# Kernel tuning notes

Hardware: AMD Instinct MI355X
Metric: run time of the kernel (lower is better)

## Reference

```python
import jax, jax.numpy as jnp
import numpy as np

B, T, E, HH, V = 64, 128, 256, 256, 50000  # HH = hidden_size // 2 per LTC level
DT = 1.0


def setup_inputs() -> dict:
    key = jax.random.key(0)
    ks = jax.random.split(key, 12)
    s_in = 1.0 / np.sqrt(E)
    s_rec = 1.0 / np.sqrt(HH)
    tokens = jax.random.randint(ks[0], (B, T), 0, V, dtype=jnp.int32)
    emb = jax.random.normal(ks[1], (V, E), jnp.float32) * 0.02
    W_in0 = jax.random.normal(ks[2], (HH, E), jnp.float32) * s_in
    W_rec0 = jax.random.normal(ks[3], (HH, HH), jnp.float32) * s_rec
    b0 = jnp.zeros((HH,), jnp.float32)
    tau0 = jax.random.uniform(ks[4], (HH,), jnp.float32)
    # NCP sparsity mask: keep prob = 1 - sparsity_level = 0.5
    mask0 = (jax.random.uniform(ks[5], (HH, HH)) > 0.5).astype(jnp.float32)
    W_in1 = jax.random.normal(ks[6], (HH, HH), jnp.float32) * s_rec
    W_rec1 = jax.random.normal(ks[7], (HH, HH), jnp.float32) * s_rec
    b1 = jnp.zeros((HH,), jnp.float32)
    tau1 = jax.random.uniform(ks[8], (HH,), jnp.float32)
    mask1 = (jax.random.uniform(ks[9], (HH, HH)) > 0.5).astype(jnp.float32)
    return {"tokens": tokens, "emb": emb,
            "W_in0": W_in0, "W_rec0": W_rec0, "b0": b0, "tau0": tau0, "mask0": mask0,
            "W_in1": W_in1, "W_rec1": W_rec1, "b1": b1, "tau1": tau1, "mask1": mask1}


def _ltc_scan(x_seq, W_in, W_rec, mask, b, tau_raw):
    """LTC Euler integration over time. x_seq: [B, T, D] -> [B, T, H]."""
    tau = jax.nn.softplus(tau_raw) + 0.1        # positive time constants [H]
    Wr = W_rec * mask                            # NCP sparse recurrent weights
    x_proj = jnp.einsum('btd,hd->bth', x_seq, W_in) + b  # precompute input drive
    h0 = jnp.zeros((x_seq.shape[0], W_rec.shape[0]), x_seq.dtype)

    def step(h, xp_t):
        pre = xp_t + h @ Wr.T
        h_new = h + DT * ((-h + jnp.tanh(pre)) / tau)
        return h_new, h_new

    _, hs = jax.lax.scan(step, h0, jnp.swapaxes(x_proj, 0, 1))  # [T, B, H]
    return jnp.swapaxes(hs, 0, 1)


def reference(tokens, emb, W_in0, W_rec0, b0, tau0, mask0,
              W_in1, W_rec1, b1, tau1, mask1):
    x = emb[tokens]                                   # [B, T, E]
    h0_seq = _ltc_scan(x, W_in0, W_rec0, mask0, b0, tau0)      # level 0: [B, T, HH]
    h1_seq = _ltc_scan(h0_seq, W_in1, W_rec1, mask1, b1, tau1)  # level 1: [B, T, HH]
    return jnp.concatenate([h0_seq, h1_seq], axis=-1)  # [B, T, 2*HH] = hidden_size
```

## Files before the change

kernel.cpp:

```cpp
#include <hip/hip_runtime.h>
#include <hip/hip_bf16.h>

#define B_ 64
#define T_ 128
#define E_ 256
#define H_ 256
#define OW_ 512
#define LP 264
#define MAGIC 0x5AD00000u

typedef unsigned short ushort_t;
typedef __attribute__((ext_vector_type(8))) short bf16x8;
typedef __attribute__((ext_vector_type(4))) float f32x4;

#define LGKM_BARRIER() asm volatile("s_waitcnt lgkmcnt(0)\n\ts_barrier" ::: "memory")
#define PIN_FRAG(x) asm volatile("" : "+v"(x))

__device__ __forceinline__ ushort_t f2bf(float f) {
    unsigned int x = __float_as_uint(f);
    unsigned int r = x + 0x7FFFu + ((x >> 16) & 1u);
    return (ushort_t)(r >> 16);
}
__device__ __forceinline__ float fast_tanh(float x) {
    float e = __expf(2.0f * x);
    return 1.0f - 2.0f * __builtin_amdgcn_rcpf(e + 1.0f);
}
__device__ __forceinline__ bf16x8 load_bfrag(const float* W, const float* M,
                                             size_t base) {
    float4 a = *(const float4*)(W + base);
    float4 b = *(const float4*)(W + base + 4);
    if (M) {
        float4 ma = *(const float4*)(M + base);
        float4 mb = *(const float4*)(M + base + 4);
        a.x *= ma.x; a.y *= ma.y; a.z *= ma.z; a.w *= ma.w;
        b.x *= mb.x; b.y *= mb.y; b.z *= mb.z; b.w *= mb.w;
    }
    union { bf16x8 v; ushort_t u[8]; } r;
    r.u[0] = f2bf(a.x); r.u[1] = f2bf(a.y); r.u[2] = f2bf(a.z); r.u[3] = f2bf(a.w);
    r.u[4] = f2bf(b.x); r.u[5] = f2bf(b.y); r.u[6] = f2bf(b.z); r.u[7] = f2bf(b.w);
    return r.v;
}

__device__ __forceinline__ int a_off(int r, int k) {
    return ((k >> 5) << 9) + (((k >> 3) & 3) << 7) + (r << 3) + (k & 7);
}

template<bool FUSE, bool WAIT>
__device__ __forceinline__ void scan_core(
    int grp, ushort_t (*hb)[4096],
    const float* xp, int xp_stride, int xp_col,
    float* hout, int out_col,
    const float* Wrec, const float* Wmask, const float* tau_raw,
    const float* Wf, const float* bfv, float* xf,
    unsigned int* flag, const unsigned int* projf)
{
    const int tid  = threadIdx.x;
    const int lane = tid & 63;
    const int wv   = tid >> 6;
    const int quad = lane >> 4;
    const int l15  = lane & 15;
    const int n0   = wv * 32;
    const int bg   = grp * 8;

    bf16x8 Bf[2][8];
    #pragma unroll
    for (int tc = 0; tc < 2; ++tc)
        #pragma unroll
        for (int kk = 0; kk < 8; ++kk)
            Bf[tc][kk] = load_bfrag(Wrec, Wmask,
                (size_t)(n0 + tc * 16 + l15) * H_ + kk * 32 + quad * 8);

    bf16x8 Bf2[2][8];
    float  b2[2] = {0.f, 0.f};
    if (FUSE) {
        #pragma unroll
        for (int tc = 0; tc < 2; ++tc) {
            b2[tc] = bfv[n0 + tc * 16 + l15];
            #pragma unroll
            for (int kk = 0; kk < 8; ++kk)
                Bf2[tc][kk] = load_bfrag(Wf, nullptr,
                    (size_t)(n0 + tc * 16 + l15) * H_ + kk * 32 + quad * 8);
        }
    }

    float inv_tau[2], h_prev[2][2];
    float xp_c[2][2], xp_n[2][2], xp_nn[2][2];
    #pragma unroll
    for (int tc = 0; tc < 2; ++tc) {
        inv_tau[tc] = 1.0f / (logf(1.0f + __expf(tau_raw[n0 + tc * 16 + l15])) + 0.1f);
        #pragma unroll
        for (int reg = 0; reg < 2; ++reg) {
            h_prev[tc][reg] = 0.0f;
            xp_c[tc][reg] = xp_n[tc][reg] = xp_nn[tc][reg] = 0.0f;
        }
    }

    int woff[2][2];
    #pragma unroll
    for (int tc = 0; tc < 2; ++tc)
        #pragma unroll
        for (int reg = 0; reg < 2; ++reg)
            woff[tc][reg] = a_off(quad * 4 + reg, n0 + tc * 16 + l15);
    const int ab = ((l15 & 2) == 0) ? (lane * 8) : 0;

    if (!WAIT) {
        if (FUSE && projf != nullptr) {
            if (tid < 8) {
                const unsigned p = (unsigned)(bg + tid);
                for (;;) {
                    unsigned v = __hip_atomic_load(&projf[p], __ATOMIC_ACQUIRE,
                                                   __HIP_MEMORY_SCOPE_AGENT);
                    if (v == MAGIC) break;
                    __builtin_amdgcn_s_sleep(2);
                }
            }
            __syncthreads();
        }
        #pragma unroll
        for (int tc = 0; tc < 2; ++tc)
            #pragma unroll
            for (int reg = 0; reg < 2; ++reg) {
                const int b = bg + quad * 2 + reg;
                const int c = n0 + tc * 16 + l15;
                xp_c[tc][reg] = xp[(size_t)(b * T_ + 0) * xp_stride + xp_col + c];
                xp_n[tc][reg] = xp[(size_t)(b * T_ + 1) * xp_stride + xp_col + c];
            }
    }

    for (int i = tid; i < 4096; i += 512)
        ((unsigned int*)&hb[0][0])[i] = 0u;
    __syncthreads();

    const int tmax = FUSE ? T_ : (T_ - 1);
    for (int t = 0; t <= tmax; ++t) {
        const int rb = t & 1;

        #pragma unroll
        for (int tc = 0; tc < 2; ++tc)
            #pragma unroll
            for (int kk = 0; kk < 8; ++kk) {
                PIN_FRAG(Bf[tc][kk]);
                if (FUSE) PIN_FRAG(Bf2[tc][kk]);
            }

        if (WAIT && t < T_ && (t & 7) == 0) {
            if (tid == 0) {
                const unsigned need = (unsigned)(t >> 3) + 1u;
                for (;;) {
                    unsigned d = __hip_atomic_load(flag, __ATOMIC_ACQUIRE,
                                                   __HIP_MEMORY_SCOPE_AGENT) - MAGIC;
                    if (d >= need && d <= 16u) break;
                    __builtin_amdgcn_s_sleep(2);
                }
            }
            __syncthreads();
            #pragma unroll
            for (int tc = 0; tc < 2; ++tc)
                #pragma unroll
                for (int reg = 0; reg < 2; ++reg) {
                    const int b = bg + quad * 2 + reg;
                    xp_c[tc][reg] = xp[(size_t)(b * T_ + t) * xp_stride + xp_col
                                       + n0 + tc * 16 + l15];
                }
        }

        bf16x8 Af[8];
        {
            const ushort_t* a0 = &hb[rb][0];
            #pragma unroll
            for (int kk = 0; kk < 8; ++kk)
                Af[kk] = *(const bf16x8*)(a0 + ab + kk * 512);
        }

        if (t < T_) {
            if (WAIT) {
                if ((t & 7) != 7 && t + 1 < T_) {
                    #pragma unroll
                    for (int tc = 0; tc < 2; ++tc)
                        #pragma unroll
                        for (int reg = 0; reg < 2; ++reg) {
                            const int b = bg + quad * 2 + reg;
                            xp_n[tc][reg] = xp[(size_t)(b * T_ + t + 1) * xp_stride
                                               + xp_col + n0 + tc * 16 + l15];
                        }
                }
            } else if (t + 2 < T_) {
                if (FUSE && projf != nullptr && ((t + 2) & 31) == 0) {
                    if (tid < 8) {
                        const unsigned p = (unsigned)(((t + 2) >> 5) * 64 + bg + tid);
                        for (;;) {
                            unsigned v = __hip_atomic_load(&projf[p],
                                                           __ATOMIC_ACQUIRE,
                                                           __HIP_MEMORY_SCOPE_AGENT);
                            if (v == MAGIC) break;
                            __builtin_amdgcn_s_sleep(2);
                        }
                    }
                    __syncthreads();
                }
                #pragma unroll
                for (int tc = 0; tc < 2; ++tc)
                    #pragma unroll
                    for (int reg = 0; reg < 2; ++reg) {
                        const int b = bg + quad * 2 + reg;
                        xp_nn[tc][reg] = xp[(size_t)(b * T_ + t + 2) * xp_stride
                                            + xp_col + n0 + tc * 16 + l15];
                    }
            }

            f32x4 acc[2] = {{0.f,0.f,0.f,0.f},{0.f,0.f,0.f,0.f}};
            #pragma unroll
            for (int kk = 0; kk < 8; ++kk)
                #pragma unroll
                for (int tc = 0; tc < 2; ++tc)
                    acc[tc] = __builtin_amdgcn_mfma_f32_16x16x32_bf16(
                        Af[kk], Bf[tc][kk], acc[tc], 0, 0, 0);

            #pragma unroll
            for (int tc = 0; tc < 2; ++tc) {
                const int c = n0 + tc * 16 + l15;
                #pragma unroll
                for (int reg = 0; reg < 2; ++reg) {
                    const int b = bg + quad * 2 + reg;
                    const float pre = xp_c[tc][reg] + acc[tc][reg];
                    const float hn  = h_prev[tc][reg]
                                    + (fast_tanh(pre) - h_prev[tc][reg]) * inv_tau[tc];
                    h_prev[tc][reg] = hn;
                    hb[rb ^ 1][woff[tc][reg]] = f2bf(hn);
                    hout[(size_t)(b * T_ + t) * OW_ + out_col + c] = hn;
                }
            }
            if (WAIT) {
                if ((t & 7) != 7) {
                    #pragma unroll
                    for (int tc = 0; tc < 2; ++tc)
                        #pragma unroll
                        for (int reg = 0; reg < 2; ++reg)
                            xp_c[tc][reg] = xp_n[tc][reg];
                }
            } else {
                #pragma unroll
                for (int tc = 0; tc < 2; ++tc)
                    #pragma unroll
                    for (int reg = 0; reg < 2; ++reg) {
                        xp_c[tc][reg] = xp_n[tc][reg];
                        xp_n[tc][reg] = xp_nn[tc][reg];
                    }
            }
        }

        if (FUSE && t > 0) {
            f32x4 acc2[2];
            #pragma unroll
            for (int tc = 0; tc < 2; ++tc)
                acc2[tc] = (f32x4){b2[tc], b2[tc], b2[tc], b2[tc]};
            #pragma unroll
            for (int kk = 0; kk < 8; ++kk)
                #pragma unroll
                for (int tc = 0; tc < 2; ++tc)
                    acc2[tc] = __builtin_amdgcn_mfma_f32_16x16x32_bf16(
                        Af[kk], Bf2[tc][kk], acc2[tc], 0, 0, 0);
            #pragma unroll
            for (int tc = 0; tc < 2; ++tc) {
                const int c = n0 + tc * 16 + l15;
                #pragma unroll
                for (int reg = 0; reg < 2; ++reg) {
                    const int b = bg + quad * 2 + reg;
                    __hip_atomic_store(&xf[(size_t)(b * T_ + t - 1) * H_ + c],
                                       acc2[tc][reg],
                                       __ATOMIC_RELAXED, __HIP_MEMORY_SCOPE_AGENT);
                }
            }
        }

        if (FUSE && t > 0 && (t & 7) == 0) {
            __syncthreads();
            if (tid == 0)
                __hip_atomic_store(flag, MAGIC + (unsigned)(t >> 3),
                                   __ATOMIC_RELEASE, __HIP_MEMORY_SCOPE_AGENT);
        } else if (t < tmax) {
            LGKM_BARRIER();
        }
    }
}

__device__ __forceinline__ void proj_body(
    int r0, const float* __restrict__ src, int src_stride, int src_col,
    const int* __restrict__ tok,
    const float* __restrict__ Wi, const float* __restrict__ bias,
    float* __restrict__ dst, int dst_stride, int dst_col,
    unsigned int* done, int done_idx)
{
    const int tid  = threadIdx.x;
    const int lane = tid & 63;
    const int wv   = tid >> 6;
    const int quad = lane >> 4;
    const int l15  = lane & 15;
    const int n0   = wv * 32;

    __shared__ __align__(16) ushort_t As[32][LP];

    bf16x8 Bf[2][8];
    float  bj[2];
    #pragma unroll
    for (int tc = 0; tc < 2; ++tc) {
        const int n = n0 + tc * 16 + l15;
        bj[tc] = bias[n];
        #pragma unroll
        for (int kk = 0; kk < 8; ++kk)
            Bf[tc][kk] = load_bfrag(Wi, nullptr, (size_t)n * H_ + kk * 32 + quad * 8);
    }

    {
        const int row = tid >> 4;
        const int seg = tid & 15;
        const size_t sb = (tok ? (size_t)tok[r0 + row] : (size_t)(r0 + row))
                          * src_stride + src_col + seg * 16;
        union { uint4 q[2]; ushort_t u[16]; } p;
        #pragma unroll
        for (int h = 0; h < 2; ++h) {
            float4 f0 = *(const float4*)(src + sb + h * 8);
            float4 f1 = *(const float4*)(src + sb + h * 8 + 4);
            p.u[h*8+0] = f2bf(f0.x); p.u[h*8+1] = f2bf(f0.y);
            p.u[h*8+2] = f2bf(f0.z); p.u[h*8+3] = f2bf(f0.w);
            p.u[h*8+4] = f2bf(f1.x); p.u[h*8+5] = f2bf(f1.y);
            p.u[h*8+6] = f2bf(f1.z); p.u[h*8+7] = f2bf(f1.w);
        }
        *(uint4*)&As[row][seg * 16]     = p.q[0];
        *(uint4*)&As[row][seg * 16 + 8] = p.q[1];
    }
    __syncthreads();

    #pragma unroll
    for (int rt = 0; rt < 2; ++rt) {
        bf16x8 Af[8];
        #pragma unroll
        for (int kk = 0; kk < 8; ++kk)
            Af[kk] = *(const bf16x8*)&As[rt * 16 + l15][kk * 32 + quad * 8];

        f32x4 acc[2] = {{bj[0],bj[0],bj[0],bj[0]}, {bj[1],bj[1],bj[1],bj[1]}};
        #pragma unroll
        for (int kk = 0; kk < 8; ++kk)
            #pragma unroll
            for (int tc = 0; tc < 2; ++tc)
                acc[tc] = __builtin_amdgcn_mfma_f32_16x16x32_bf16(
                    Af[kk], Bf[tc][kk], acc[tc], 0, 0, 0);

        #pragma unroll
        for (int tc = 0; tc < 2; ++tc) {
            const int c = n0 + tc * 16 + l15;
            #pragma unroll
            for (int reg = 0; reg < 4; ++reg) {
                const int r = r0 + rt * 16 + quad * 4 + reg;
                if (done)
                    __hip_atomic_store(&dst[(size_t)r * dst_stride + dst_col + c],
                                       acc[tc][reg],
                                       __ATOMIC_RELAXED, __HIP_MEMORY_SCOPE_AGENT);
                else
                    dst[(size_t)r * dst_stride + dst_col + c] = acc[tc][reg];
            }
        }
    }

    if (done) {
        __syncthreads();
        if (tid == 0)
            __hip_atomic_store(&done[done_idx], MAGIC,
                               __ATOMIC_RELEASE, __HIP_MEMORY_SCOPE_AGENT);
    }
}

__global__ __launch_bounds__(512, 1)
void ltc_all(const int* __restrict__ tokens, const float* __restrict__ emb,
             const float* __restrict__ Wi0, const float* __restrict__ b0v,
             const float* __restrict__ Wr0, const float* __restrict__ m0,
             const float* __restrict__ t0,
             const float* __restrict__ Wi1, const float* __restrict__ b1v,
             const float* __restrict__ Wr1, const float* __restrict__ m1,
             const float* __restrict__ t1,
             float* out, float* xf, unsigned int* flags, unsigned int* projf)
{
    __shared__ __align__(16) ushort_t hb[2][4096];
    if (blockIdx.x < 8)
        scan_core<true, false>(blockIdx.x, hb,
                               out, OW_, H_,
                               out, 0,
                               Wr0, m0, t0, Wi1, b1v, xf,
                               flags + blockIdx.x, projf);
    else if (blockIdx.x < 16)
        scan_core<false, true>(blockIdx.x - 8, hb,
                               xf, H_, 0,
                               out, H_,
                               Wr1, m1, t1, nullptr, nullptr, nullptr,
                               flags + blockIdx.x - 8, nullptr);
    else {
        const int p  = blockIdx.x - 16;
        const int r0 = (p & 63) * T_ + (p >> 6) * 32;
        proj_body(r0, emb, E_, 0, tokens, Wi0, b0v, out, OW_, H_, projf, p);
    }
}

__global__ __launch_bounds__(512, 1)
void ltc_dual(float* out,
              const float* __restrict__ Wr0, const float* __restrict__ m0,
              const float* __restrict__ t0,
              const float* __restrict__ Wi1, const float* __restrict__ b1v,
              const float* __restrict__ Wr1, const float* __restrict__ m1,
              const float* __restrict__ t1,
              float* xf, unsigned int* flags)
{
    __shared__ __align__(16) ushort_t hb[2][4096];
    if (blockIdx.x < 8)
        scan_core<true, false>(blockIdx.x, hb,
                               out, OW_, H_, out, 0,
                               Wr0, m0, t0, Wi1, b1v, xf,
                               flags + blockIdx.x, nullptr);
    else
        scan_core<false, true>(blockIdx.x - 8, hb,
                               xf, H_, 0, out, H_,
                               Wr1, m1, t1, nullptr, nullptr, nullptr,
                               flags + blockIdx.x - 8, nullptr);
}

__global__ __launch_bounds__(512, 1)
void ltc_single(const float* xp, int xp_stride, int xp_col,
                float* hout, int out_col,
                const float* __restrict__ Wr, const float* __restrict__ mk,
                const float* __restrict__ tu)
{
    __shared__ __align__(16) ushort_t hb[2][4096];
    scan_core<false, false>(blockIdx.x, hb, xp, xp_stride, xp_col,
                            hout, out_col, Wr, mk, tu,
                            nullptr, nullptr, nullptr, nullptr, nullptr);
}

__global__ __launch_bounds__(512, 2)
void proj_mfma(const float* __restrict__ src, int src_stride, int src_col,
               const int* __restrict__ tok,
               const float* __restrict__ Wi,
               const float* __restrict__ bias,
               float* __restrict__ dst, int dst_stride, int dst_col)
{
    proj_body(blockIdx.x * 32, src, src_stride, src_col, tok, Wi, bias,
              dst, dst_stride, dst_col, nullptr, 0);
}

extern "C" void kernel_launch(void* const* d_in, const int* in_sizes, int n_in,
                              void* d_out, int out_size, void* d_ws, size_t ws_size,
                              hipStream_t stream)
{
    const int*   tokens = (const int*)d_in[0];
    const float* emb    = (const float*)d_in[1];
    const float* W_in0  = (const float*)d_in[2];
    const float* W_rec0 = (const float*)d_in[3];
    const float* b0     = (const float*)d_in[4];
    const float* tau0   = (const float*)d_in[5];
    const float* mask0  = (const float*)d_in[6];
    const float* W_in1  = (const float*)d_in[7];
    const float* W_rec1 = (const float*)d_in[8];
    const float* b1     = (const float*)d_in[9];
    const float* tau1   = (const float*)d_in[10];
    const float* mask1  = (const float*)d_in[11];
    float* out = (float*)d_out;
    (void)in_sizes; (void)n_in; (void)out_size;

    const size_t xf_elems = (size_t)B_ * T_ * H_;
    const size_t xf_bytes = xf_elems * sizeof(float);

    if (ws_size >= xf_bytes + 64 + 1024) {
        float* xf = (float*)d_ws;
        unsigned int* flags = (unsigned int*)((char*)d_ws + xf_bytes);
        unsigned int* projf = (unsigned int*)((char*)d_ws + xf_bytes + 64);
        ltc_all<<<dim3(272), dim3(512), 0, stream>>>(
            tokens, emb, W_in0, b0, W_rec0, mask0, tau0,
            W_in1, b1, W_rec1, mask1, tau1, out, xf, flags, projf);
    } else if (ws_size >= xf_bytes + 64) {
        float* xf = (float*)d_ws;
        unsigned int* flags = (unsigned int*)((char*)d_ws + xf_bytes);
        proj_mfma<<<dim3(256), dim3(512), 0, stream>>>(
            emb, E_, 0, tokens, W_in0, b0, out, OW_, H_);
        ltc_dual<<<dim3(16), dim3(512), 0, stream>>>(
            out, W_rec0, mask0, tau0, W_in1, b1, W_rec1, mask1, tau1, xf, flags);
    } else {
        proj_mfma<<<dim3(256), dim3(512), 0, stream>>>(
            emb, E_, 0, tokens, W_in0, b0, out, OW_, H_);
        ltc_single<<<dim3(8), dim3(512), 0, stream>>>(
            out, OW_, H_, out, 0, W_rec0, mask0, tau0);
        proj_mfma<<<dim3(256), dim3(512), 0, stream>>>(
            out, OW_, 0, nullptr, W_in1, b1, out, OW_, H_);
        ltc_single<<<dim3(8), dim3(512), 0, stream>>>(
            out, OW_, H_, out, H_, W_rec1, mask1, tau1);
    }
}
```

Baseline: 262.2 us.

## Move level-1 input projection from level-0 scan into dedicated fuser blocks

The level-0 scan blocks no longer compute the W_in1 projection inline each timestep. Eight new fuser blocks wait for 8-step chunks of h0 and project them with MFMA into xf, which the level-1 scan then consumes. The embedding projection is also re-chunked so the first 8 timesteps are published first, letting the level-0 scan start sooner. This shortens the serial per-step critical path of the level-0 recurrence, at the cost of extra flag handshakes and re-reading h0 from global memory.

```diff
diff --git a/kernel.cpp b/kernel.cpp
--- a/kernel.cpp
+++ b/kernel.cpp
@@ -45,13 +45,12 @@
     return ((k >> 5) << 9) + (((k >> 3) & 3) << 7) + (r << 3) + (k & 7);
 }
 
-template<bool FUSE, bool WAIT>
+template<bool PUB, bool WAIT>
 __device__ __forceinline__ void scan_core(
     int grp, ushort_t (*hb)[4096],
     const float* xp, int xp_stride, int xp_col,
     float* hout, int out_col,
     const float* Wrec, const float* Wmask, const float* tau_raw,
-    const float* Wf, const float* bfv, float* xf,
     unsigned int* flag, const unsigned int* projf)
 {
     const int tid  = threadIdx.x;
@@ -70,19 +69,6 @@
             Bf[tc][kk] = load_bfrag(Wrec, Wmask,
                 (size_t)(n0 + tc * 16 + l15) * H_ + kk * 32 + quad * 8);
 
-    bf16x8 Bf2[2][8];
-    float  b2[2] = {0.f, 0.f};
-    if (FUSE) {
-        #pragma unroll
-        for (int tc = 0; tc < 2; ++tc) {
-            b2[tc] = bfv[n0 + tc * 16 + l15];
-            #pragma unroll
-            for (int kk = 0; kk < 8; ++kk)
-                Bf2[tc][kk] = load_bfrag(Wf, nullptr,
-                    (size_t)(n0 + tc * 16 + l15) * H_ + kk * 32 + quad * 8);
-        }
-    }
-
     float inv_tau[2], h_prev[2][2];
     float xp_c[2][2], xp_n[2][2], xp_nn[2][2];
     #pragma unroll
@@ -104,11 +90,11 @@
     const int ab = ((l15 & 2) == 0) ? (lane * 8) : 0;
 
     if (!WAIT) {
-        if (FUSE && projf != nullptr) {
+        if (PUB && projf != nullptr) {
             if (tid < 8) {
-                const unsigned p = (unsigned)(bg + tid);
                 for (;;) {
-                    unsigned v = __hip_atomic_load(&projf[p], __ATOMIC_ACQUIRE,
+                    unsigned v = __hip_atomic_load(&projf[bg + tid],
+                                                   __ATOMIC_ACQUIRE,
                                                    __HIP_MEMORY_SCOPE_AGENT);
                     if (v == MAGIC) break;
                     __builtin_amdgcn_s_sleep(2);
@@ -131,19 +117,16 @@
         ((unsigned int*)&hb[0][0])[i] = 0u;
     __syncthreads();
 
-    const int tmax = FUSE ? T_ : (T_ - 1);
-    for (int t = 0; t <= tmax; ++t) {
+    for (int t = 0; t < T_; ++t) {
         const int rb = t & 1;
 
         #pragma unroll
         for (int tc = 0; tc < 2; ++tc)
             #pragma unroll
-            for (int kk = 0; kk < 8; ++kk) {
+            for (int kk = 0; kk < 8; ++kk)
                 PIN_FRAG(Bf[tc][kk]);
-                if (FUSE) PIN_FRAG(Bf2[tc][kk]);
-            }
-
-        if (WAIT && t < T_ && (t & 7) == 0) {
+
+        if (WAIT && (t & 7) == 0) {
             if (tid == 0) {
                 const unsigned need = (unsigned)(t >> 3) + 1u;
                 for (;;) {
@@ -172,24 +155,26 @@
                 Af[kk] = *(const bf16x8*)(a0 + ab + kk * 512);
         }
 
-        if (t < T_) {
-            if (WAIT) {
-                if ((t & 7) != 7 && t + 1 < T_) {
+        if (WAIT) {
+            if ((t & 7) != 7 && t + 1 < T_) {
+                #pragma unroll
+                for (int tc = 0; tc < 2; ++tc)
                     #pragma unroll
-                    for (int tc = 0; tc < 2; ++tc)
-                        #pragma unroll
-                        for (int reg = 0; reg < 2; ++reg) {
-                            const int b = bg + quad * 2 + reg;
-                            xp_n[tc][reg] = xp[(size_t)(b * T_ + t + 1) * xp_stride
-                                               + xp_col + n0 + tc * 16 + l15];
-                        }
-                }
-            } else if (t + 2 < T_) {
-                if (FUSE && projf != nullptr && ((t + 2) & 31) == 0) {
+                    for (int reg = 0; reg < 2; ++reg) {
+                        const int b = bg + quad * 2 + reg;
+                        xp_n[tc][reg] = xp[(size_t)(b * T_ + t + 1) * xp_stride
+                                           + xp_col + n0 + tc * 16 + l15];
+                    }
+            }
+        } else if (t + 2 < T_) {
+            if (PUB && projf != nullptr) {
+                const int tp2 = t + 2;
+                const int w = (tp2 == 8) ? 1 : (tp2 == 32) ? 2
+                            : (tp2 == 64) ? 3 : (tp2 == 96) ? 4 : -1;
+                if (w >= 0) {
                     if (tid < 8) {
-                        const unsigned p = (unsigned)(((t + 2) >> 5) * 64 + bg + tid);
                         for (;;) {
-                            unsigned v = __hip_atomic_load(&projf[p],
+                            unsigned v = __hip_atomic_load(&projf[w * 64 + bg + tid],
                                                            __ATOMIC_ACQUIRE,
                                                            __HIP_MEMORY_SCOPE_AGENT);
                             if (v == MAGIC) break;
@@ -198,98 +183,78 @@
                     }
                     __syncthreads();
                 }
+            }
+            #pragma unroll
+            for (int tc = 0; tc < 2; ++tc)
+                #pragma unroll
+                for (int reg = 0; reg < 2; ++reg) {
+                    const int b = bg + quad * 2 + reg;
+                    xp_nn[tc][reg] = xp[(size_t)(b * T_ + t + 2) * xp_stride
+                                        + xp_col + n0 + tc * 16 + l15];
+                }
+        }
+
+        f32x4 acc[2] = {{0.f,0.f,0.f,0.f},{0.f,0.f,0.f,0.f}};
+        #pragma unroll
+        for (int kk = 0; kk < 8; ++kk)
+            #pragma unroll
+            for (int tc = 0; tc < 2; ++tc)
+                acc[tc] = __builtin_amdgcn_mfma_f32_16x16x32_bf16(
+                    Af[kk], Bf[tc][kk], acc[tc], 0, 0, 0);
+
+        #pragma unroll
+        for (int tc = 0; tc < 2; ++tc) {
+            const int c = n0 + tc * 16 + l15;
+            #pragma unroll
+            for (int reg = 0; reg < 2; ++reg) {
+                const int b = bg + quad * 2 + reg;
+                const float pre = xp_c[tc][reg] + acc[tc][reg];
+                const float hn  = h_prev[tc][reg]
+                                + (fast_tanh(pre) - h_prev[tc][reg]) * inv_tau[tc];
+                h_prev[tc][reg] = hn;
+                hb[rb ^ 1][woff[tc][reg]] = f2bf(hn);
+                if (PUB)
+                    __hip_atomic_store(&hout[(size_t)(b * T_ + t) * OW_ + out_col + c],
+                                       hn, __ATOMIC_RELAXED, __HIP_MEMORY_SCOPE_AGENT);
+                else
+                    hout[(size_t)(b * T_ + t) * OW_ + out_col + c] = hn;
+            }
+        }
+        if (WAIT) {
+            if ((t & 7) != 7) {
                 #pragma unroll
                 for (int tc = 0; tc < 2; ++tc)
                     #pragma unroll
-                    for (int reg = 0; reg < 2; ++reg) {
-                        const int b = bg + quad * 2 + reg;
-                        xp_nn[tc][reg] = xp[(size_t)(b * T_ + t + 2) * xp_stride
-                                            + xp_col + n0 + tc * 16 + l15];
-                    }
-            }
-
-            f32x4 acc[2] = {{0.f,0.f,0.f,0.f},{0.f,0.f,0.f,0.f}};
-            #pragma unroll
-            for (int kk = 0; kk < 8; ++kk)
-                #pragma unroll
-                for (int tc = 0; tc < 2; ++tc)
-                    acc[tc] = __builtin_amdgcn_mfma_f32_16x16x32_bf16(
-                        Af[kk], Bf[tc][kk], acc[tc], 0, 0, 0);
-
-            #pragma unroll
-            for (int tc = 0; tc < 2; ++tc) {
-                const int c = n0 + tc * 16 + l15;
+                    for (int reg = 0; reg < 2; ++reg)
+                        xp_c[tc][reg] = xp_n[tc][reg];
+            }
+        } else {
+            #pragma unroll
+            for (int tc = 0; tc < 2; ++tc)
                 #pragma unroll
                 for (int reg = 0; reg < 2; ++reg) {
-                    const int b = bg + quad * 2 + reg;
-                    const float pre = xp_c[tc][reg] + acc[tc][reg];
-                    const float hn  = h_prev[tc][reg]
-                                    + (fast_tanh(pre) - h_prev[tc][reg]) * inv_tau[tc];
-                    h_prev[tc][reg] = hn;
-                    hb[rb ^ 1][woff[tc][reg]] = f2bf(hn);
-                    hout[(size_t)(b * T_ + t) * OW_ + out_col + c] = hn;
-                }
-            }
-            if (WAIT) {
-                if ((t & 7) != 7) {
-                    #pragma unroll
-                    for (int tc = 0; tc < 2; ++tc)
-                        #pragma unroll
-                        for (int reg = 0; reg < 2; ++reg)
-                            xp_c[tc][reg] = xp_n[tc][reg];
-                }
-            } else {
-                #pragma unroll
-                for (int tc = 0; tc < 2; ++tc)
-                    #pragma unroll
-                    for (int reg = 0; reg < 2; ++reg) {
-                        xp_c[tc][reg] = xp_n[tc][reg];
-                        xp_n[tc][reg] = xp_nn[tc][reg];
-                    }
-            }
-        }
-
-        if (FUSE && t > 0) {
-            f32x4 acc2[2];
-            #pragma unroll
-            for (int tc = 0; tc < 2; ++tc)
-                acc2[tc] = (f32x4){b2[tc], b2[tc], b2[tc], b2[tc]};
-            #pragma unroll
-            for (int kk = 0; kk < 8; ++kk)
-                #pragma unroll
-                for (int tc = 0; tc < 2; ++tc)
-                    acc2[tc] = __builtin_amdgcn_mfma_f32_16x16x32_bf16(
-                        Af[kk], Bf2[tc][kk], acc2[tc], 0, 0, 0);
-            #pragma unroll
-            for (int tc = 0; tc < 2; ++tc) {
-                const int c = n0 + tc * 16 + l15;
-                #pragma unroll
-                for (int reg = 0; reg < 2; ++reg) {
-                    const int b = bg + quad * 2 + reg;
-                    __hip_atomic_store(&xf[(size_t)(b * T_ + t - 1) * H_ + c],
-                                       acc2[tc][reg],
-                                       __ATOMIC_RELAXED, __HIP_MEMORY_SCOPE_AGENT);
-                }
-            }
-        }
-
-        if (FUSE && t > 0 && (t & 7) == 0) {
+                    xp_c[tc][reg] = xp_n[tc][reg];
+                    xp_n[tc][reg] = xp_nn[tc][reg];
+                }
+        }
+
+        if (PUB && (t & 7) == 7) {
             __syncthreads();
             if (tid == 0)
-                __hip_atomic_store(flag, MAGIC + (unsigned)(t >> 3),
+                __hip_atomic_store(flag, MAGIC + (unsigned)((t >> 3) + 1),
                                    __ATOMIC_RELEASE, __HIP_MEMORY_SCOPE_AGENT);
-        } else if (t < tmax) {
+        } else if (t + 1 < T_) {
             LGKM_BARRIER();
         }
     }
 }
 
-__device__ __forceinline__ void proj_body(
-    int r0, const float* __restrict__ src, int src_stride, int src_col,
-    const int* __restrict__ tok,
-    const float* __restrict__ Wi, const float* __restrict__ bias,
-    float* __restrict__ dst, int dst_stride, int dst_col,
-    unsigned int* done, int done_idx)
+__device__ __forceinline__ void fuser_core(
+    int grp, ushort_t (*As)[LP],
+    const float* __restrict__ hsrc,
+    const float* __restrict__ Wi1, const float* __restrict__ b1v,
+    float* __restrict__ xf,
+    const unsigned int* flagP, unsigned int* flagF)
 {
     const int tid  = threadIdx.x;
     const int lane = tid & 63;
@@ -297,8 +262,106 @@
     const int quad = lane >> 4;
     const int l15  = lane & 15;
     const int n0   = wv * 32;
-
-    __shared__ __align__(16) ushort_t As[32][LP];
+    const int bg   = grp * 8;
+
+    bf16x8 Bf[2][8];
+    float  bj[2];
+    #pragma unroll
+    for (int tc = 0; tc < 2; ++tc) {
+        const int c = n0 + tc * 16 + l15;
+        bj[tc] = b1v[c];
+        #pragma unroll
+        for (int kk = 0; kk < 8; ++kk)
+            Bf[tc][kk] = load_bfrag(Wi1, nullptr,
+                                    (size_t)c * H_ + kk * 32 + quad * 8);
+    }
+
+    const int srow = tid >> 3;
+    const int sseg = tid & 7;
+    const int sb   = bg + (srow >> 3);
+
+    for (int c = 1; c <= 16; ++c) {
+        if (tid == 0) {
+            for (;;) {
+                unsigned d = __hip_atomic_load(flagP, __ATOMIC_ACQUIRE,
+                                               __HIP_MEMORY_SCOPE_AGENT) - MAGIC;
+                if (d >= (unsigned)c && d <= 16u) break;
+                __builtin_amdgcn_s_sleep(2);
+            }
+        }
+        __syncthreads();
+        const int t0 = (c - 1) * 8;
+
+        {
+            const float* srcp = hsrc
+                + (size_t)(sb * T_ + t0 + (srow & 7)) * OW_ + sseg * 32;
+            union { uint4 q[4]; ushort_t u[32]; } pk;
+            #pragma unroll
+            for (int h = 0; h < 4; ++h) {
+                float4 f0 = *(const float4*)(srcp + h * 8);
+                float4 f1 = *(const float4*)(srcp + h * 8 + 4);
+                pk.u[h*8+0] = f2bf(f0.x); pk.u[h*8+1] = f2bf(f0.y);
+                pk.u[h*8+2] = f2bf(f0.z); pk.u[h*8+3] = f2bf(f0.w);
+                pk.u[h*8+4] = f2bf(f1.x); pk.u[h*8+5] = f2bf(f1.y);
+                pk.u[h*8+6] = f2bf(f1.z); pk.u[h*8+7] = f2bf(f1.w);
+            }
+            #pragma unroll
+            for (int h = 0; h < 4; ++h)
+                *(uint4*)&As[srow][sseg * 32 + h * 8] = pk.q[h];
+        }
+        __syncthreads();
+
+        #pragma unroll
+        for (int rt = 0; rt < 4; ++rt) {
+            bf16x8 Af[8];
+            #pragma unroll
+            for (int kk = 0; kk < 8; ++kk)
+                Af[kk] = *(const bf16x8*)&As[rt * 16 + l15][kk * 32 + quad * 8];
+
+            f32x4 acc[2] = {{bj[0],bj[0],bj[0],bj[0]},
+                            {bj[1],bj[1],bj[1],bj[1]}};
+            #pragma unroll
+            for (int kk = 0; kk < 8; ++kk)
+                #pragma unroll
+                for (int tc = 0; tc < 2; ++tc)
+                    acc[tc] = __builtin_amdgcn_mfma_f32_16x16x32_bf16(
+                        Af[kk], Bf[tc][kk], acc[tc], 0, 0, 0);
+
+            #pragma unroll
+            for (int tc = 0; tc < 2; ++tc) {
+                const int cc = n0 + tc * 16 + l15;
+                #pragma unroll
+                for (int reg = 0; reg < 4; ++reg) {
+                    const int r  = rt * 16 + quad * 4 + reg;
+                    const int b  = bg + (r >> 3);
+                    const int tt = t0 + (r & 7);
+                    __hip_atomic_store(&xf[(size_t)(b * T_ + tt) * H_ + cc],
+                                       acc[tc][reg],
+                                       __ATOMIC_RELAXED, __HIP_MEMORY_SCOPE_AGENT);
+                }
+            }
+        }
+        __syncthreads();
+        if (tid == 0)
+            __hip_atomic_store(flagF, MAGIC + (unsigned)c,
+                               __ATOMIC_RELEASE, __HIP_MEMORY_SCOPE_AGENT);
+    }
+}
+
+__device__ __forceinline__ void proj_body(
+    ushort_t (*As)[LP], int r0, int nrows,
+    const float* __restrict__ src, int src_stride, int src_col,
+    const int* __restrict__ tok,
+    const float* __restrict__ Wi, const float* __restrict__ bias,
+    float* __restrict__ dst, int dst_stride, int dst_col,
+    unsigned int* done, int done_idx)
+{
+    const int tid  = threadIdx.x;
+    const int lane = tid & 63;
+    const int wv   = tid >> 6;
+    const int quad = lane >> 4;
+    const int l15  = lane & 15;
+    const int n0   = wv * 32;
 
     bf16x8 Bf[2][8];
     float  bj[2];
@@ -314,25 +377,28 @@
     {
         const int row = tid >> 4;
         const int seg = tid & 15;
-        const size_t sb = (tok ? (size_t)tok[r0 + row] : (size_t)(r0 + row))
-                          * src_stride + src_col + seg * 16;
-        union { uint4 q[2]; ushort_t u[16]; } p;
-        #pragma unroll
-        for (int h = 0; h < 2; ++h) {
-            float4 f0 = *(const float4*)(src + sb + h * 8);
-            float4 f1 = *(const float4*)(src + sb + h * 8 + 4);
-            p.u[h*8+0] = f2bf(f0.x); p.u[h*8+1] = f2bf(f0.y);
-            p.u[h*8+2] = f2bf(f0.z); p.u[h*8+3] = f2bf(f0.w);
-            p.u[h*8+4] = f2bf(f1.x); p.u[h*8+5] = f2bf(f1.y);
-            p.u[h*8+6] = f2bf(f1.z); p.u[h*8+7] = f2bf(f1.w);
-        }
-        *(uint4*)&As[row][seg * 16]     = p.q[0];
-        *(uint4*)&As[row][seg * 16 + 8] = p.q[1];
+        if (row < nrows) {
+            const size_t sb = (tok ? (size_t)tok[r0 + row] : (size_t)(r0 + row))
+                              * src_stride + src_col + seg * 16;
+            union { uint4 q[2]; ushort_t u[16]; } p;
+            #pragma unroll
+            for (int h = 0; h < 2; ++h) {
+                float4 f0 = *(const float4*)(src + sb + h * 8);
+                float4 f1 = *(const float4*)(src + sb + h * 8 + 4);
+                p.u[h*8+0] = f2bf(f0.x); p.u[h*8+1] = f2bf(f0.y);
+                p.u[h*8+2] = f2bf(f0.z); p.u[h*8+3] = f2bf(f0.w);
+                p.u[h*8+4] = f2bf(f1.x); p.u[h*8+5] = f2bf(f1.y);
+                p.u[h*8+6] = f2bf(f1.z); p.u[h*8+7] = f2bf(f1.w);
+            }
+            *(uint4*)&As[row][seg * 16]     = p.q[0];
+            *(uint4*)&As[row][seg * 16 + 8] = p.q[1];
+        }
     }
     __syncthreads();
 
     #pragma unroll
     for (int rt = 0; rt < 2; ++rt) {
+        if (rt * 16 >= nrows) break;
         bf16x8 Af[8];
         #pragma unroll
         for (int kk = 0; kk < 8; ++kk)
@@ -351,13 +417,16 @@
             const int c = n0 + tc * 16 + l15;
             #pragma unroll
             for (int reg = 0; reg < 4; ++reg) {
-                const int r = r0 + rt * 16 + quad * 4 + reg;
-                if (done)
-                    __hip_atomic_store(&dst[(size_t)r * dst_stride + dst_col + c],
-                                       acc[tc][reg],
-                                       __ATOMIC_RELAXED, __HIP_MEMORY_SCOPE_AGENT);
-                else
-                    dst[(size_t)r * dst_stride + dst_col + c] = acc[tc][reg];
+                const int rl = rt * 16 + quad * 4 + reg;
+                if (rl < nrows) {
+                    const int r = r0 + rl;
+                    if (done)
+                        __hip_atomic_store(&dst[(size_t)r * dst_stride + dst_col + c],
+                                           acc[tc][reg],
+                                           __ATOMIC_RELAXED, __HIP_MEMORY_SCOPE_AGENT);
+                    else
+                        dst[(size_t)r * dst_stride + dst_col + c] = acc[tc][reg];
+                }
             }
         }
     }
@@ -374,52 +443,35 @@
 void ltc_all(const int* __restrict__ tokens, const float* __restrict__ emb,
              const float* __restrict__ Wi0, const float* __restrict__ b0v,
              const float* __restrict__ Wr0, const float* __restrict__ m0,
-             const float* __restrict__ t0,
+             const float* __restrict__ t0v,
              const float* __restrict__ Wi1, const float* __restrict__ b1v,
              const float* __restrict__ Wr1, const float* __restrict__ m1,
-             const float* __restrict__ t1,
-             float* out, float* xf, unsigned int* flags, unsigned int* projf)
-{
-    __shared__ __align__(16) ushort_t hb[2][4096];
+             const float* __restrict__ t1v,
+             float* out, float* xf,
+             unsigned int* flagsP, unsigned int* flagsF, unsigned int* projf)
+{
+    __shared__ __align__(16) ushort_t smem[64][LP];
     if (blockIdx.x < 8)
-        scan_core<true, false>(blockIdx.x, hb,
+        scan_core<true, false>(blockIdx.x, (ushort_t(*)[4096])&smem[0][0],
                                out, OW_, H_,
                                out, 0,
-                               Wr0, m0, t0, Wi1, b1v, xf,
-                               flags + blockIdx.x, projf);
+                               Wr0, m0, t0v, flagsP + blockIdx.x, projf);
     else if (blockIdx.x < 16)
-        scan_core<false, true>(blockIdx.x - 8, hb,
+        scan_core<false, true>(blockIdx.x - 8, (ushort_t(*)[4096])&smem[0][0],
                                xf, H_, 0,
                                out, H_,
-                               Wr1, m1, t1, nullptr, nullptr, nullptr,
-                               flags + blockIdx.x - 8, nullptr);
+                               Wr1, m1, t1v, flagsF + (blockIdx.x - 8), nullptr);
+    else if (blockIdx.x < 24)
+        fuser_core(blockIdx.x - 16, smem, out, Wi1, b1v, xf,
+                   flagsP + (blockIdx.x - 16), flagsF + (blockIdx.x - 16));
     else {
-        const int p  = blockIdx.x - 16;
-        const int r0 = (p & 63) * T_ + (p >> 6) * 32;
-        proj_body(r0, emb, E_, 0, tokens, Wi0, b0v, out, OW_, H_, projf, p);
-    }
-}
-
-__global__ __launch_bounds__(512, 1)
-void ltc_dual(float* out,
-              const float* __restrict__ Wr0, const float* __restrict__ m0,
-              const float* __restrict__ t0,
-              const float* __restrict__ Wi1, const float* __restrict__ b1v,
-              const float* __restrict__ Wr1, const float* __restrict__ m1,
-              const float* __restrict__ t1,
-              float* xf, unsigned int* flags)
-{
-    __shared__ __align__(16) ushort_t hb[2][4096];
-    if (blockIdx.x < 8)
-        scan_core<true, false>(blockIdx.x, hb,
-                               out, OW_, H_, out, 0,
-                               Wr0, m0, t0, Wi1, b1v, xf,
-                               flags + blockIdx.x, nullptr);
-    else
-        scan_core<false, true>(blockIdx.x - 8, hb,
-                               xf, H_, 0, out, H_,
-                               Wr1, m1, t1, nullptr, nullptr, nullptr,
-                               flags + blockIdx.x - 8, nullptr);
+        const int p = blockIdx.x - 24;
+        const int w = p >> 6, b = p & 63;
+        const int r0 = b * T_ + (w == 0 ? 0 : (w == 1 ? 8 : 32 * (w - 1)));
+        const int nr = (w == 0 ? 8 : (w == 1 ? 24 : 32));
+        proj_body((ushort_t(*)[LP])smem, r0, nr, emb, E_, 0, tokens,
+                  Wi0, b0v, out, OW_, H_, projf, p);
+    }
 }
 
 __global__ __launch_bounds__(512, 1)
@@ -430,8 +482,7 @@
 {
     __shared__ __align__(16) ushort_t hb[2][4096];
     scan_core<false, false>(blockIdx.x, hb, xp, xp_stride, xp_col,
-                            hout, out_col, Wr, mk, tu,
-                            nullptr, nullptr, nullptr, nullptr, nullptr);
+                            hout, out_col, Wr, mk, tu, nullptr, nullptr);
 }
 
 __global__ __launch_bounds__(512, 2)
@@ -441,7 +492,8 @@
                const float* __restrict__ bias,
                float* __restrict__ dst, int dst_stride, int dst_col)
 {
-    proj_body(blockIdx.x * 32, src, src_stride, src_col, tok, Wi, bias,
+    __shared__ __align__(16) ushort_t As[32][LP];
+    proj_body(As, blockIdx.x * 32, 32, src, src_stride, src_col, tok, Wi, bias,
               dst, dst_stride, dst_col, nullptr, 0);
 }
 
@@ -464,23 +516,17 @@
     float* out = (float*)d_out;
     (void)in_sizes; (void)n_in; (void)out_size;
 
-    const size_t xf_elems = (size_t)B_ * T_ * H_;
-    const size_t xf_bytes = xf_elems * sizeof(float);
-
-    if (ws_size >= xf_bytes + 64 + 1024) {
+    const size_t xf_bytes = (size_t)B_ * T_ * H_ * sizeof(float);
+    const size_t need = xf_bytes + 64 + 64 + 320 * sizeof(unsigned int);
+
+    if (ws_size >= need) {
         float* xf = (float*)d_ws;
-        unsigned int* flags = (unsigned int*)((char*)d_ws + xf_bytes);
-        unsigned int* projf = (unsigned int*)((char*)d_ws + xf_bytes + 64);
-        ltc_all<<<dim3(272), dim3(512), 0, stream>>>(
+        unsigned int* flagsP = (unsigned int*)((char*)d_ws + xf_bytes);
+        unsigned int* flagsF = (unsigned int*)((char*)d_ws + xf_bytes + 64);
+        unsigned int* projf  = (unsigned int*)((char*)d_ws + xf_bytes + 128);
+        ltc_all<<<dim3(344), dim3(512), 0, stream>>>(
             tokens, emb, W_in0, b0, W_rec0, mask0, tau0,
-            W_in1, b1, W_rec1, mask1, tau1, out, xf, flags, projf);
-    } else if (ws_size >= xf_bytes + 64) {
-        float* xf = (float*)d_ws;
-        unsigned int* flags = (unsigned int*)((char*)d_ws + xf_bytes);
-        proj_mfma<<<dim3(256), dim3(512), 0, stream>>>(
-            emb, E_, 0, tokens, W_in0, b0, out, OW_, H_);
-        ltc_dual<<<dim3(16), dim3(512), 0, stream>>>(
-            out, W_rec0, mask0, tau0, W_in1, b1, W_rec1, mask1, tau1, xf, flags);
+            W_in1, b1, W_rec1, mask1, tau1, out, xf, flagsP, flagsF, projf);
     } else {
         proj_mfma<<<dim3(256), dim3(512), 0, stream>>>(
             emb, E_, 0, tokens, W_in0, b0, out, OW_, H_);
```

Result: faster. 234.9 us (-10.4%).
